# Kernel optimization log

Measured on AMD Instinct MI355X. Metric: run time of the kernel, lower is better.

Reference implementation:

```python
import jax, jax.numpy as jnp
import numpy as np

N = 50000      # nodes
E = 800000     # edges
IN_CH = 32
H = 64         # hidden_channels
OUT_CH = 16
L = 4          # num_layers
EPS = 1e-7     # GENConv message eps
LN_EPS = 1e-5


def _lin(key, fan_in, fan_out):
    kw, kb = jax.random.split(key)
    s = 1.0 / np.sqrt(fan_in)
    W = jax.random.uniform(kw, (fan_in, fan_out), jnp.float32, -s, s)
    b = jax.random.uniform(kb, (fan_out,), jnp.float32, -s, s)
    return W, b


def setup_inputs() -> dict:
    key = jax.random.key(0)
    ks = jax.random.split(key, 8)
    x = jax.random.normal(ks[0], (N, IN_CH), jnp.float32)
    edge_index = jax.random.randint(ks[1], (2, E), 0, N, dtype=jnp.int32)
    node_W, node_b = _lin(ks[2], IN_CH, H)
    W1, b1, W2, b2 = [], [], [], []
    for i in range(L):
        w1, bb1 = _lin(jax.random.fold_in(ks[3], i), H, 2 * H)
        w2, bb2 = _lin(jax.random.fold_in(ks[4], i), 2 * H, H)
        W1.append(w1); b1.append(bb1); W2.append(w2); b2.append(bb2)
    inp = {
        "x": x,
        "node_W": node_W, "node_b": node_b,
        "W1": jnp.stack(W1), "b1": jnp.stack(b1),          # [L,H,2H],[L,2H]
        "mlp_ln_g": jnp.ones((L, 2 * H), jnp.float32),      # LayerNorm inside GENConv MLP
        "mlp_ln_b": jnp.zeros((L, 2 * H), jnp.float32),
        "W2": jnp.stack(W2), "b2": jnp.stack(b2),          # [L,2H,H],[L,H]
        "t": jnp.ones((L,), jnp.float32),                   # learnable softmax temperature
        "ln_g": jnp.ones((L, H), jnp.float32),              # DeepGCNLayer LayerNorms
        "ln_b": jnp.zeros((L, H), jnp.float32),
        "edge_index": edge_index,
    }
    gW, gb = _lin(ks[5], H, OUT_CH)
    nW, nb = _lin(ks[6], H, OUT_CH + 1)
    inp.update({"g_W": gW, "g_b": gb, "n_W": nW, "n_b": nb})
    return inp


def _layer_norm(h, g, b):
    mu = h.mean(-1, keepdims=True)
    var = ((h - mu) ** 2).mean(-1, keepdims=True)
    return (h - mu) * jax.lax.rsqrt(var + LN_EPS) * g + b


def _gen_conv(h, src, dst, W1, b1, lg, lb, W2, b2, t):
    # message: relu(x_j) + eps  -> [E, H]
    m = jax.nn.relu(h[src]) + EPS
    # per-destination, per-channel scatter softmax with temperature t
    z = t * m
    zmax = jax.ops.segment_max(z, dst, num_segments=N)
    zmax = jnp.where(jnp.isfinite(zmax), zmax, 0.0)  # empty segments -> -inf
    a = jnp.exp(z - zmax[dst])
    denom = jax.ops.segment_sum(a, dst, num_segments=N)
    agg = jax.ops.segment_sum(m * a, dst, num_segments=N) / jnp.maximum(denom, EPS)
    out = agg + h  # root add
    # MLP [H, 2H, H] with LayerNorm + ReLU between
    u = jax.nn.relu(_layer_norm(out @ W1 + b1, lg, lb))
    return u @ W2 + b2


def reference(x, node_W, node_b, W1, b1, mlp_ln_g, mlp_ln_b, W2, b2, t,
              ln_g, ln_b, g_W, g_b, n_W, n_b, edge_index):
    src, dst = edge_index[0], edge_index[1]
    h = x @ node_W + node_b  # node encoder
    # first layer: conv only
    h = _gen_conv(h, src, dst, W1[0], b1[0], mlp_ln_g[0], mlp_ln_b[0], W2[0], b2[0], t[0])
    # remaining res+ blocks: x + conv(relu(norm(x)))  (dropout identity in eval)
    for i in range(1, L):
        y = jax.nn.relu(_layer_norm(h, ln_g[i], ln_b[i]))
        h = h + _gen_conv(y, src, dst, W1[i], b1[i], mlp_ln_g[i], mlp_ln_b[i], W2[i], b2[i], t[i])
    h = jax.nn.relu(_layer_norm(h, ln_g[0], ln_b[0]))
    g_out = jnp.max(h @ g_W + g_b, axis=0)   # batch=None -> global max over nodes
    n_out = h @ n_W + n_b
    return g_out, n_out
```

## Files before the change

kernel.cpp:

```cpp
#include <hip/hip_runtime.h>

#define NN 50000
#define NE 800000
#define INC 32
#define HH 64
#define H2 128
#define OC 16
#define ON 17
#define NL 4
#define MEPS 1e-7f
#define LNE 1e-5f
#define SCAN_BLOCKS 196
#define NLB ((NN + 127) / 128)
#define NBW ((NL * H2 * HH + 255) / 256)
#define NBH ((NE + 255) / 256)
#define NBE ((NN + 3) / 4)

typedef __attribute__((ext_vector_type(8))) short bf16x8;
typedef __attribute__((ext_vector_type(4))) float f32x4;

__device__ __forceinline__ unsigned short f2b(float x) {
    unsigned b = __float_as_uint(x);
    b += 0x7FFFu + ((b >> 16) & 1u);
    return (unsigned short)(b >> 16);
}
__device__ __forceinline__ float b2f(unsigned short u) {
    return __uint_as_float(((unsigned)u) << 16);
}

__global__ __launch_bounds__(256) void k_pre(
    const float* __restrict__ W1, const float* __restrict__ W2,
    const float* __restrict__ nW, const float* __restrict__ gW,
    const float* __restrict__ nbp, const float* __restrict__ gb,
    unsigned short* __restrict__ w1h, unsigned short* __restrict__ w1l,
    unsigned short* __restrict__ w2h, unsigned short* __restrict__ w2l,
    unsigned short* __restrict__ whh, unsigned short* __restrict__ whl,
    float* __restrict__ bc,
    const int* __restrict__ edst, int* __restrict__ counts, int* __restrict__ rank,
    const float* __restrict__ x, const float* __restrict__ nodeW,
    const float* __restrict__ nodeB, float* __restrict__ h,
    unsigned short* __restrict__ hbf)
{
    __shared__ float Ws[INC * HH];
    __shared__ float bs[HH];
    int bid = blockIdx.x, tid = threadIdx.x;
    if (bid < NBW) {
        int i = bid * 256 + tid;
        if (i < 48 * 64) {
            int j = i >> 6, k = i & 63;
            float v = 0.f;
            if (j < ON) v = nW[k * ON + j];
            else if (j < 33) v = gW[k * OC + (j - ON)];
            unsigned short hi = f2b(v);
            whh[i] = hi;
            whl[i] = f2b(v - b2f(hi));
        }
        if (i < 48) bc[i] = (i < ON) ? nbp[i] : ((i < 33) ? gb[i - ON] : 0.f);
        if (i >= NL * H2 * HH) return;
        int l = i / (H2 * HH), r = i % (H2 * HH);
        {
            int c = r / HH, k = r % HH;
            float v = W1[(size_t)l * HH * H2 + (size_t)k * H2 + c];
            unsigned short hi = f2b(v);
            w1h[i] = hi;
            w1l[i] = f2b(v - b2f(hi));
        }
        {
            int c = r / H2, k = r % H2;
            float v = W2[(size_t)l * H2 * HH + (size_t)k * HH + c];
            unsigned short hi = f2b(v);
            w2h[i] = hi;
            w2l[i] = f2b(v - b2f(hi));
        }
        return;
    }
    if (bid < NBW + NBH) {
        int e = (bid - NBW) * 256 + tid;
        if (e < NE) rank[e] = atomicAdd(&counts[edst[e]], 1);
        return;
    }
    for (int i = tid; i < INC * HH; i += 256) Ws[i] = nodeW[i];
    if (tid < HH) bs[tid] = nodeB[tid];
    __syncthreads();
    int wid = tid >> 6, lane = tid & 63;
    int n = (bid - NBW - NBH) * 4 + wid;
    if (n >= NN) return;
    float v = (lane < INC) ? x[(size_t)n * INC + lane] : 0.f;
    float acc = bs[lane];
    #pragma unroll
    for (int k = 0; k < INC; ++k)
        acc += __shfl(v, k) * Ws[k * HH + lane];
    h[(size_t)n * HH + lane] = acc;
    hbf[(size_t)n * HH + lane] = f2b(acc);
}

__global__ __launch_bounds__(256) void k_scan1(const int* __restrict__ counts,
                                               int* __restrict__ incl, int* __restrict__ bsums) {
    __shared__ int s[256];
    int t = threadIdx.x;
    int i = blockIdx.x * 256 + t;
    int v = (i < NN) ? counts[i] : 0;
    s[t] = v;
    __syncthreads();
    for (int off = 1; off < 256; off <<= 1) {
        int x = (t >= off) ? s[t - off] : 0;
        __syncthreads();
        s[t] += x;
        __syncthreads();
    }
    if (i < NN) incl[i] = s[t];
    if (t == 255) bsums[blockIdx.x] = s[255];
}

__global__ __launch_bounds__(256) void k_scan23(const int* __restrict__ counts,
                                                int* __restrict__ rowst, const int* __restrict__ bsums,
                                                int2* __restrict__ meta) {
    __shared__ int s[256];
    int t = threadIdx.x;
    int v = (t < SCAN_BLOCKS) ? bsums[t] : 0;
    s[t] = v;
    __syncthreads();
    for (int off = 1; off < 256; off <<= 1) {
        int x = (t >= off) ? s[t - off] : 0;
        __syncthreads();
        s[t] += x;
        __syncthreads();
    }
    int ex = s[t] - v;
    __syncthreads();
    s[t] = ex;
    __syncthreads();
    int pref = s[blockIdx.x];
    int i = blockIdx.x * 256 + t;
    if (i < NN) {
        int st = rowst[i] - counts[i] + pref;
        rowst[i] = st;
        meta[i] = make_int2(st, counts[i]);
    }
}

__global__ __launch_bounds__(256) void k_scatter2(const int* __restrict__ src, const int* __restrict__ dst,
                                                  const int* __restrict__ rank, const int* __restrict__ rowst,
                                                  int* __restrict__ ssrc) {
    int e = blockIdx.x * 256 + threadIdx.x;
    if (e < NE) ssrc[rowst[dst[e]] + rank[e]] = src[e];
}

__global__ __launch_bounds__(512, 4) void k_layer(
    const float* __restrict__ yin, const unsigned short* __restrict__ ybf_in,
    const int2* __restrict__ meta, const int* __restrict__ ssrc, const float* __restrict__ tp,
    const unsigned short* __restrict__ w1h, const unsigned short* __restrict__ w1l,
    const float* __restrict__ b1,
    const float* __restrict__ mlg, const float* __restrict__ mlb,
    const unsigned short* __restrict__ w2h, const unsigned short* __restrict__ w2l,
    const float* __restrict__ b2,
    const float* __restrict__ hres, float* __restrict__ hout,
    const float* __restrict__ lng1, const float* __restrict__ lnb1,
    float* __restrict__ yout, unsigned short* __restrict__ ybf_out,
    const float* __restrict__ lngF, const float* __restrict__ lnbF,
    const unsigned short* __restrict__ whh, const unsigned short* __restrict__ whl,
    const float* __restrict__ bc, float* __restrict__ dout, float* __restrict__ gmax)
{
    __shared__ __align__(16) unsigned short R1[2 * 128 * 68];
    __shared__ __align__(16) unsigned short R2[2 * 128 * 72];
    __shared__ float smax[8][16];
    unsigned short* aghS = R1;
    unsigned short* aglS = R1 + 128 * 68;
    unsigned short* W2hS = R1;
    unsigned short* W2lS = R1 + 128 * 68;
    bool last = (lng1 == nullptr);
    int tid = threadIdx.x;
    int w = tid >> 6, lane = tid & 63;
    int nl = lane & 15, g = lane >> 4;
    int nodeM = blockIdx.x * 128 + w * 16 + nl;
    bool validM = nodeM < NN;
    float tval = *tp;

    #pragma unroll
    for (int it = 0; it < 2; ++it) {
        int c = tid + it * 512;
        int row = c >> 3, col = (c & 7) << 3;
        float4 vh = *(const float4*)(w1h + c * 8);
        float4 vl = *(const float4*)(w1l + c * 8);
        *(float4*)&R2[row * 72 + col] = vh;
        *(float4*)&R2[9216 + row * 72 + col] = vl;
    }

    {
        int half = lane >> 5, l = lane & 31;
        for (int p = 0; p < 8; ++p) {
            int ln = p * 16 + w * 2 + half;
            int n = blockIdx.x * 128 + ln;
            bool valid = n < NN;
            int2 m = valid ? meta[n] : make_int2(0, 0);
            int start = m.x, deg = m.y;
            int dA = __shfl(deg, 0), dB = __shfl(deg, 32);
            int dmax = max(dA, dB);
            float Sa0 = 0.f, Sm0 = 0.f, Sa1 = 0.f, Sm1 = 0.f;
            for (int win = 0; win < dmax; win += 64) {
                int wcnt = min(64, dmax - win);
                int idxLo = (win + l < deg) ? ssrc[start + win + l] : 0;
                int idxHi = (win + 32 + l < deg) ? ssrc[start + win + 32 + l] : 0;
                for (int e0 = 0; e0 < wcnt; e0 += 8) {
                    float c0[8], c1[8];
                    int ev[8];
                    #pragma unroll
                    for (int i = 0; i < 8; ++i) {
                        int e = e0 + i;
                        ev[i] = win + e;
                        int sel = (e < 32) ? idxLo : idxHi;
                        int s = __shfl(sel, (lane & 32) | (e & 31));
                        unsigned vv = *(const unsigned*)(ybf_in + (size_t)s * HH + l * 2);
                        c0[i] = b2f((unsigned short)(vv & 0xffffu));
                        c1[i] = b2f((unsigned short)(vv >> 16));
                    }
                    #pragma unroll
                    for (int i = 0; i < 8; ++i) {
                        bool ok = ev[i] < deg;
                        float m0 = fmaxf(c0[i], 0.f) + MEPS;
                        float m1 = fmaxf(c1[i], 0.f) + MEPS;
                        float a0 = ok ? __expf(tval * m0) : 0.f;
                        float a1 = ok ? __expf(tval * m1) : 0.f;
                        Sa0 += a0; Sm0 += m0 * a0;
                        Sa1 += a1; Sm1 += m1 * a1;
                    }
                }
            }
            float av0 = 0.f, av1 = 0.f;
            if (valid) {
                float2 yv = *(const float2*)(yin + (size_t)n * HH + l * 2);
                av0 = Sm0 / fmaxf(Sa0, MEPS) + yv.x;
                av1 = Sm1 / fmaxf(Sa1, MEPS) + yv.y;
            }
            unsigned short h0 = f2b(av0), h1 = f2b(av1);
            ushort2 ph = {h0, h1};
            ushort2 pl = {f2b(av0 - b2f(h0)), f2b(av1 - b2f(h1))};
            *(ushort2*)&aghS[ln * 68 + 2 * l] = ph;
            *(ushort2*)&aglS[ln * 68 + 2 * l] = pl;
        }
    }
    __syncthreads();

    int lnM = w * 16 + nl;
    bf16x8 bAh[2], bAl[2];
    #pragma unroll
    for (int kc = 0; kc < 2; ++kc) {
        bAh[kc] = *(const bf16x8*)&aghS[lnM * 68 + kc * 32 + g * 8];
        bAl[kc] = *(const bf16x8*)&aglS[lnM * 68 + kc * 32 + g * 8];
    }
    f32x4 accU[8];
    #pragma unroll
    for (int t = 0; t < 8; ++t) {
        int uc = t * 16 + g * 4;
        float4 bb = *(const float4*)(b1 + uc);
        f32x4 a = {bb.x, bb.y, bb.z, bb.w};
        #pragma unroll
        for (int kc = 0; kc < 2; ++kc) {
            int wo = (t * 16 + nl) * 72 + kc * 32 + g * 8;
            bf16x8 ah = *(const bf16x8*)&R2[wo];
            bf16x8 al = *(const bf16x8*)&R2[9216 + wo];
            a = __builtin_amdgcn_mfma_f32_16x16x32_bf16(ah, bAh[kc], a, 0, 0, 0);
            a = __builtin_amdgcn_mfma_f32_16x16x32_bf16(al, bAh[kc], a, 0, 0, 0);
            a = __builtin_amdgcn_mfma_f32_16x16x32_bf16(ah, bAl[kc], a, 0, 0, 0);
        }
        accU[t] = a;
    }

    float s = 0.f, sq = 0.f;
    #pragma unroll
    for (int t = 0; t < 8; ++t) {
        #pragma unroll
        for (int j = 0; j < 4; ++j) { float v = accU[t][j]; s += v; sq += v * v; }
    }
    s += __shfl_xor(s, 16); sq += __shfl_xor(sq, 16);
    s += __shfl_xor(s, 32); sq += __shfl_xor(sq, 32);
    float mu = s * (1.f / 128.f);
    float var = sq * (1.f / 128.f) - mu * mu;
    float rs = rsqrtf(fmaxf(var, 0.f) + LNE);

    __syncthreads();

    #pragma unroll
    for (int it = 0; it < 2; ++it) {
        int c = tid + it * 512;
        int row = c >> 4, col = (c & 15) << 3;
        float4 vh = *(const float4*)(w2h + c * 8);
        float4 vl = *(const float4*)(w2l + c * 8);
        *(float4*)&W2hS[row * 136 + col] = vh;
        *(float4*)&W2lS[row * 136 + col] = vl;
    }
    unsigned short* myUt = R2 + w * (16 * 136);
    #pragma unroll
    for (int t = 0; t < 8; ++t) {
        int uc = t * 16 + g * 4;
        float4 gg = *(const float4*)(mlg + uc);
        float4 bb = *(const float4*)(mlb + uc);
        ushort4 pk;
        pk.x = f2b(fmaxf((accU[t][0] - mu) * rs * gg.x + bb.x, 0.f));
        pk.y = f2b(fmaxf((accU[t][1] - mu) * rs * gg.y + bb.y, 0.f));
        pk.z = f2b(fmaxf((accU[t][2] - mu) * rs * gg.z + bb.z, 0.f));
        pk.w = f2b(fmaxf((accU[t][3] - mu) * rs * gg.w + bb.w, 0.f));
        *(ushort4*)(&myUt[nl * 136 + uc]) = pk;
    }
    __syncthreads();

    bf16x8 bB[4];
    #pragma unroll
    for (int kc = 0; kc < 4; ++kc)
        bB[kc] = *(const bf16x8*)(&myUt[nl * 136 + kc * 32 + g * 8]);
    f32x4 accO[4];
    #pragma unroll
    for (int ot = 0; ot < 4; ++ot) {
        int oc = ot * 16 + g * 4;
        float4 bb = *(const float4*)(b2 + oc);
        f32x4 a = {bb.x, bb.y, bb.z, bb.w};
        #pragma unroll
        for (int kc = 0; kc < 4; ++kc) {
            int wo = (ot * 16 + nl) * 136 + kc * 32 + g * 8;
            bf16x8 ah = *(const bf16x8*)&W2hS[wo];
            bf16x8 al = *(const bf16x8*)&W2lS[wo];
            a = __builtin_amdgcn_mfma_f32_16x16x32_bf16(ah, bB[kc], a, 0, 0, 0);
            a = __builtin_amdgcn_mfma_f32_16x16x32_bf16(al, bB[kc], a, 0, 0, 0);
        }
        accO[ot] = a;
    }

    float4 oo[4];
    #pragma unroll
    for (int ot = 0; ot < 4; ++ot) {
        int oc = ot * 16 + g * 4;
        float4 o;
        o.x = accO[ot][0]; o.y = accO[ot][1]; o.z = accO[ot][2]; o.w = accO[ot][3];
        if (validM && hres) {
            float4 hr = *(const float4*)(hres + (size_t)nodeM * HH + oc);
            o.x += hr.x; o.y += hr.y; o.z += hr.z; o.w += hr.w;
        }
        oo[ot] = o;
    }

    if (!last) {
        #pragma unroll
        for (int ot = 0; ot < 4; ++ot) {
            int oc = ot * 16 + g * 4;
            if (validM) *(float4*)(hout + (size_t)nodeM * HH + oc) = oo[ot];
        }
        float s2 = 0.f, sq2 = 0.f;
        #pragma unroll
        for (int ot = 0; ot < 4; ++ot) {
            s2 += oo[ot].x + oo[ot].y + oo[ot].z + oo[ot].w;
            sq2 += oo[ot].x * oo[ot].x + oo[ot].y * oo[ot].y
                 + oo[ot].z * oo[ot].z + oo[ot].w * oo[ot].w;
        }
        s2 += __shfl_xor(s2, 16); sq2 += __shfl_xor(sq2, 16);
        s2 += __shfl_xor(s2, 32); sq2 += __shfl_xor(sq2, 32);
        float mu2 = s2 * (1.f / 64.f);
        float var2 = sq2 * (1.f / 64.f) - mu2 * mu2;
        float rs2 = rsqrtf(fmaxf(var2, 0.f) + LNE);
        #pragma unroll
        for (int ot = 0; ot < 4; ++ot) {
            int oc = ot * 16 + g * 4;
            float4 gg = *(const float4*)(lng1 + oc);
            float4 bb = *(const float4*)(lnb1 + oc);
            float4 v;
            v.x = fmaxf((oo[ot].x - mu2) * rs2 * gg.x + bb.x, 0.f);
            v.y = fmaxf((oo[ot].y - mu2) * rs2 * gg.y + bb.y, 0.f);
            v.z = fmaxf((oo[ot].z - mu2) * rs2 * gg.z + bb.z, 0.f);
            v.w = fmaxf((oo[ot].w - mu2) * rs2 * gg.w + bb.w, 0.f);
            if (validM) {
                *(float4*)(yout + (size_t)nodeM * HH + oc) = v;
                ushort4 p;
                p.x = f2b(v.x); p.y = f2b(v.y); p.z = f2b(v.z); p.w = f2b(v.w);
                *(ushort4*)(ybf_out + (size_t)nodeM * HH + oc) = p;
            }
        }
        return;
    }

    float s2 = 0.f, sq2 = 0.f;
    #pragma unroll
    for (int ot = 0; ot < 4; ++ot) {
        s2 += oo[ot].x + oo[ot].y + oo[ot].z + oo[ot].w;
        sq2 += oo[ot].x * oo[ot].x + oo[ot].y * oo[ot].y
             + oo[ot].z * oo[ot].z + oo[ot].w * oo[ot].w;
    }
    s2 += __shfl_xor(s2, 16); sq2 += __shfl_xor(sq2, 16);
    s2 += __shfl_xor(s2, 32); sq2 += __shfl_xor(sq2, 32);
    float mu2 = s2 * (1.f / 64.f);
    float var2 = sq2 * (1.f / 64.f) - mu2 * mu2;
    float rs2 = rsqrtf(fmaxf(var2, 0.f) + LNE);

    union { bf16x8 v; unsigned short u[8]; } Bh[2], Bl[2];
    #pragma unroll
    for (int kc = 0; kc < 2; ++kc) {
        #pragma unroll
        for (int e = 0; e < 8; ++e) {
            int ot = kc * 2 + (e >> 2);
            int c = ot * 16 + g * 4 + (e & 3);
            float hv = (e & 3) == 0 ? oo[ot].x : ((e & 3) == 1 ? oo[ot].y : ((e & 3) == 2 ? oo[ot].z : oo[ot].w));
            float v = fmaxf((hv - mu2) * rs2 * lngF[c] + lnbF[c], 0.f);
            unsigned short hi = f2b(v);
            Bh[kc].u[e] = hi;
            Bl[kc].u[e] = f2b(v - b2f(hi));
        }
    }
    f32x4 acc[3];
    #pragma unroll
    for (int t = 0; t < 3; ++t) {
        int j0 = t * 16 + g * 4;
        float4 bb = *(const float4*)(bc + j0);
        f32x4 a = {bb.x, bb.y, bb.z, bb.w};
        #pragma unroll
        for (int kc = 0; kc < 2; ++kc) {
            union { bf16x8 v; unsigned short u[8]; } Ah, Al;
            #pragma unroll
            for (int e = 0; e < 8; ++e) {
                int ot = kc * 2 + (e >> 2);
                int c = ot * 16 + g * 4 + (e & 3);
                Ah.u[e] = whh[(size_t)(t * 16 + nl) * 64 + c];
                Al.u[e] = whl[(size_t)(t * 16 + nl) * 64 + c];
            }
            a = __builtin_amdgcn_mfma_f32_16x16x32_bf16(Ah.v, Bh[kc].v, a, 0, 0, 0);
            a = __builtin_amdgcn_mfma_f32_16x16x32_bf16(Al.v, Bh[kc].v, a, 0, 0, 0);
            a = __builtin_amdgcn_mfma_f32_16x16x32_bf16(Ah.v, Bl[kc].v, a, 0, 0, 0);
        }
        acc[t] = a;
    }

    #pragma unroll
    for (int t = 0; t < 3; ++t) {
        #pragma unroll
        for (int reg = 0; reg < 4; ++reg) {
            int j = t * 16 + g * 4 + reg;
            float val = acc[t][reg];
            if (j < ON) {
                if (validM) dout[OC + (size_t)nodeM * ON + j] = val;
            } else if (j < 33) {
                float gv = validM ? val : -INFINITY;
                #pragma unroll
                for (int m = 1; m < 16; m <<= 1) gv = fmaxf(gv, __shfl_xor(gv, m));
                if (nl == 0) smax[w][j - ON] = gv;
            }
        }
    }
    __syncthreads();
    if (tid < 16) {
        float mm = -INFINITY;
        #pragma unroll
        for (int ww = 0; ww < 8; ++ww) mm = fmaxf(mm, smax[ww][tid]);
        gmax[(size_t)blockIdx.x * 16 + tid] = mm;
    }
}

__global__ void k_gdec(const float* __restrict__ gmax, float* __restrict__ dout) {
    int lane = threadIdx.x & 63;
    int ch = lane & 15, grp = lane >> 4;
    float m = -INFINITY;
    for (int b = grp; b < NLB; b += 4) m = fmaxf(m, gmax[(size_t)b * 16 + ch]);
    m = fmaxf(m, __shfl_xor(m, 16));
    m = fmaxf(m, __shfl_xor(m, 32));
    if (lane < 16) dout[ch] = m;
}

extern "C" void kernel_launch(void* const* d_in, const int* in_sizes, int n_in,
                              void* d_out, int out_size, void* d_ws, size_t ws_size,
                              hipStream_t stream) {
    const float* x     = (const float*)d_in[0];
    const float* nodeW = (const float*)d_in[1];
    const float* nodeB = (const float*)d_in[2];
    const float* W1    = (const float*)d_in[3];
    const float* b1    = (const float*)d_in[4];
    const float* mlg   = (const float*)d_in[5];
    const float* mlb   = (const float*)d_in[6];
    const float* W2    = (const float*)d_in[7];
    const float* b2    = (const float*)d_in[8];
    const float* tt    = (const float*)d_in[9];
    const float* lng   = (const float*)d_in[10];
    const float* lnb   = (const float*)d_in[11];
    const int*   ei    = (const int*)d_in[12];
    const float* gW    = (const float*)d_in[13];
    const float* gb    = (const float*)d_in[14];
    const float* nW    = (const float*)d_in[15];
    const float* nbp   = (const float*)d_in[16];
    float* out = (float*)d_out;

    char* ws = (char*)d_ws;
    size_t off = 0;
    auto alloc = [&](size_t bytes) -> void* {
        void* p = ws + off;
        off = (off + bytes + 255) & ~(size_t)255;
        return p;
    };
    int* counts    = (int*)alloc((size_t)NN * 4);
    size_t zero_end = off;
    float* gmax = (float*)alloc((size_t)NLB * 16 * 4);
    int* bsums = (int*)alloc(1024);
    int* rowst = (int*)alloc((size_t)NN * 4);
    int2* meta = (int2*)alloc((size_t)NN * 8);
    int* ssrc  = (int*)alloc((size_t)NE * 4);
    float* h   = (float*)alloc((size_t)NN * HH * 4);
    float* y   = (float*)alloc((size_t)NN * HH * 4);
    unsigned short* ybf0 = (unsigned short*)alloc((size_t)NN * HH * 2);
    unsigned short* ybf1 = (unsigned short*)alloc((size_t)NN * HH * 2);
    unsigned short* w1h = (unsigned short*)alloc((size_t)NL * H2 * HH * 2);
    unsigned short* w1l = (unsigned short*)alloc((size_t)NL * H2 * HH * 2);
    unsigned short* w2h = (unsigned short*)alloc((size_t)NL * H2 * HH * 2);
    unsigned short* w2l = (unsigned short*)alloc((size_t)NL * H2 * HH * 2);
    unsigned short* whh = (unsigned short*)alloc((size_t)48 * 64 * 2);
    unsigned short* whl = (unsigned short*)alloc((size_t)48 * 64 * 2);
    float* bc = (float*)alloc(48 * 4);
    int* rank = (int*)ybf1;

    const int* esrc = ei;
    const int* edst = ei + NE;

    hipMemsetAsync(d_ws, 0, zero_end, stream);

    k_pre<<<NBW + NBH + NBE, 256, 0, stream>>>(W1, W2, nW, gW, nbp, gb,
                                               w1h, w1l, w2h, w2l, whh, whl, bc,
                                               edst, counts, rank,
                                               x, nodeW, nodeB, h, ybf0);
    k_scan1<<<SCAN_BLOCKS, 256, 0, stream>>>(counts, rowst, bsums);
    k_scan23<<<SCAN_BLOCKS, 256, 0, stream>>>(counts, rowst, bsums, meta);
    k_scatter2<<<(NE + 255) / 256, 256, 0, stream>>>(esrc, edst, rank, rowst, ssrc);

    unsigned short* bufs[2] = {ybf0, ybf1};
    for (int l = 0; l < NL; ++l) {
        const float* yin = (l == 0) ? h : y;
        unsigned short* bin = bufs[l & 1];
        unsigned short* bout = bufs[(l + 1) & 1];
        bool lastL = (l == NL - 1);
        const float* ln1g = lastL ? nullptr : (lng + (size_t)(l + 1) * HH);
        const float* ln1b = lastL ? nullptr : (lnb + (size_t)(l + 1) * HH);
        k_layer<<<NLB, 512, 0, stream>>>(yin, bin, meta, ssrc, tt + l,
                                         w1h + (size_t)l * H2 * HH, w1l + (size_t)l * H2 * HH,
                                         b1 + (size_t)l * H2,
                                         mlg + (size_t)l * H2, mlb + (size_t)l * H2,
                                         w2h + (size_t)l * H2 * HH, w2l + (size_t)l * H2 * HH,
                                         b2 + (size_t)l * HH,
                                         (l == 0) ? (const float*)nullptr : h, h,
                                         ln1g, ln1b, y, bout,
                                         lng, lnb, whh, whl, bc, out, gmax);
    }
    k_gdec<<<1, 64, 0, stream>>>(gmax, out);
}
```

Before: 424.3 us.

## Split fused layer kernel into separate aggregation and MLP kernels

Each layer's fused gather-softmax-aggregate plus MLP kernel is split in two. A small-block aggregation kernel writes the hi/lo bf16 split of agg+root to global buffers, and an MLP kernel reads them back. The aim is higher occupancy and better latency hiding for the irregular gather, which is no longer tied to the 512-thread, LDS-heavy MLP block. The cost is an extra global round trip of the aggregated features, one more launch per layer, and a single ybf buffer instead of ping-pong.

```diff
diff --git a/kernel.cpp b/kernel.cpp
--- a/kernel.cpp
+++ b/kernel.cpp
@@ -11,7 +11,7 @@
 #define MEPS 1e-7f
 #define LNE 1e-5f
 #define SCAN_BLOCKS 196
-#define NLB ((NN + 127) / 128)
+#define NMB ((NN + 127) / 128)
 #define NBW ((NL * H2 * HH + 255) / 256)
 #define NBH ((NE + 255) / 256)
 #define NBE ((NN + 3) / 4)
@@ -146,9 +146,72 @@
     if (e < NE) ssrc[rowst[dst[e]] + rank[e]] = src[e];
 }
 
-__global__ __launch_bounds__(512, 4) void k_layer(
-    const float* __restrict__ yin, const unsigned short* __restrict__ ybf_in,
-    const int2* __restrict__ meta, const int* __restrict__ ssrc, const float* __restrict__ tp,
+__global__ __launch_bounds__(256) void k_agg(const float* __restrict__ y,
+                                             const unsigned short* __restrict__ ybf,
+                                             const int2* __restrict__ meta,
+                                             const int* __restrict__ ssrc,
+                                             const float* __restrict__ tp,
+                                             unsigned short* __restrict__ agh,
+                                             unsigned short* __restrict__ agl) {
+    int tid = threadIdx.x;
+    int w = tid >> 6, lane = tid & 63;
+    int half = lane >> 5;
+    int l = lane & 31;
+    int col = l;
+    int n = blockIdx.x * 8 + w * 2 + half;
+    bool valid = n < NN;
+    float tval = *tp;
+    int2 m = valid ? meta[n] : make_int2(0, 0);
+    int start = m.x, deg = m.y;
+
+    int dA = __shfl(deg, 0), dB = __shfl(deg, 32);
+    int dmax = max(dA, dB);
+
+    float Sa0 = 0.f, Sm0 = 0.f, Sa1 = 0.f, Sm1 = 0.f;
+    for (int win = 0; win < dmax; win += 64) {
+        int wcnt = min(64, dmax - win);
+        int idxLo = (win + l < deg) ? ssrc[start + win + l] : 0;
+        int idxHi = (win + 32 + l < deg) ? ssrc[start + win + 32 + l] : 0;
+        for (int e0 = 0; e0 < wcnt; e0 += 8) {
+            float c0[8], c1[8];
+            int ev[8];
+            #pragma unroll
+            for (int i = 0; i < 8; ++i) {
+                int e = e0 + i;
+                ev[i] = win + e;
+                int sel = (e < 32) ? idxLo : idxHi;
+                int s = __shfl(sel, (lane & 32) | (e & 31));
+                unsigned v = *(const unsigned*)(ybf + (size_t)s * HH + col * 2);
+                c0[i] = b2f((unsigned short)(v & 0xffffu));
+                c1[i] = b2f((unsigned short)(v >> 16));
+            }
+            #pragma unroll
+            for (int i = 0; i < 8; ++i) {
+                bool ok = ev[i] < deg;
+                float m0 = fmaxf(c0[i], 0.f) + MEPS;
+                float m1 = fmaxf(c1[i], 0.f) + MEPS;
+                float a0 = ok ? __expf(tval * m0) : 0.f;
+                float a1 = ok ? __expf(tval * m1) : 0.f;
+                Sa0 += a0; Sm0 += m0 * a0;
+                Sa1 += a1; Sm1 += m1 * a1;
+            }
+        }
+    }
+    if (!valid) return;
+    float agg0 = Sm0 / fmaxf(Sa0, MEPS);
+    float agg1 = Sm1 / fmaxf(Sa1, MEPS);
+    float2 yv = *(const float2*)(y + (size_t)n * HH + col * 2);
+    float av0 = agg0 + yv.x;
+    float av1 = agg1 + yv.y;
+    unsigned short h0 = f2b(av0), h1 = f2b(av1);
+    ushort2 ph = {h0, h1};
+    ushort2 pl = {f2b(av0 - b2f(h0)), f2b(av1 - b2f(h1))};
+    *(ushort2*)(agh + (size_t)n * HH + col * 2) = ph;
+    *(ushort2*)(agl + (size_t)n * HH + col * 2) = pl;
+}
+
+__global__ __launch_bounds__(512, 4) void k_mlp(
+    const unsigned short* __restrict__ agh, const unsigned short* __restrict__ agl,
     const unsigned short* __restrict__ w1h, const unsigned short* __restrict__ w1l,
     const float* __restrict__ b1,
     const float* __restrict__ mlg, const float* __restrict__ mlb,
@@ -156,25 +219,36 @@
     const float* __restrict__ b2,
     const float* __restrict__ hres, float* __restrict__ hout,
     const float* __restrict__ lng1, const float* __restrict__ lnb1,
-    float* __restrict__ yout, unsigned short* __restrict__ ybf_out,
+    float* __restrict__ y, unsigned short* __restrict__ ybf,
     const float* __restrict__ lngF, const float* __restrict__ lnbF,
     const unsigned short* __restrict__ whh, const unsigned short* __restrict__ whl,
     const float* __restrict__ bc, float* __restrict__ dout, float* __restrict__ gmax)
 {
-    __shared__ __align__(16) unsigned short R1[2 * 128 * 68];
-    __shared__ __align__(16) unsigned short R2[2 * 128 * 72];
+    __shared__ __align__(16) unsigned short W1S[2 * 128 * 72];
+    __shared__ __align__(16) unsigned short W2hS[64 * 136];
+    __shared__ __align__(16) unsigned short W2lS[64 * 136];
     __shared__ float smax[8][16];
-    unsigned short* aghS = R1;
-    unsigned short* aglS = R1 + 128 * 68;
-    unsigned short* W2hS = R1;
-    unsigned short* W2lS = R1 + 128 * 68;
     bool last = (lng1 == nullptr);
     int tid = threadIdx.x;
     int w = tid >> 6, lane = tid & 63;
     int nl = lane & 15, g = lane >> 4;
-    int nodeM = blockIdx.x * 128 + w * 16 + nl;
-    bool validM = nodeM < NN;
-    float tval = *tp;
+    int node = blockIdx.x * 128 + w * 16 + nl;
+    bool valid = node < NN;
+
+    bf16x8 bAh[2], bAl[2];
+    {
+        bf16x8 z = {0, 0, 0, 0, 0, 0, 0, 0};
+        if (valid) {
+            const unsigned short* rp = agh + (size_t)node * HH + g * 8;
+            bAh[0] = *(const bf16x8*)rp;
+            bAh[1] = *(const bf16x8*)(rp + 32);
+            const unsigned short* rq = agl + (size_t)node * HH + g * 8;
+            bAl[0] = *(const bf16x8*)rq;
+            bAl[1] = *(const bf16x8*)(rq + 32);
+        } else {
+            bAh[0] = z; bAh[1] = z; bAl[0] = z; bAl[1] = z;
+        }
+    }
 
     #pragma unroll
     for (int it = 0; it < 2; ++it) {
@@ -182,104 +256,9 @@
         int row = c >> 3, col = (c & 7) << 3;
         float4 vh = *(const float4*)(w1h + c * 8);
         float4 vl = *(const float4*)(w1l + c * 8);
-        *(float4*)&R2[row * 72 + col] = vh;
-        *(float4*)&R2[9216 + row * 72 + col] = vl;
-    }
-
-    {
-        int half = lane >> 5, l = lane & 31;
-        for (int p = 0; p < 8; ++p) {
-            int ln = p * 16 + w * 2 + half;
-            int n = blockIdx.x * 128 + ln;
-            bool valid = n < NN;
-            int2 m = valid ? meta[n] : make_int2(0, 0);
-            int start = m.x, deg = m.y;
-            int dA = __shfl(deg, 0), dB = __shfl(deg, 32);
-            int dmax = max(dA, dB);
-            float Sa0 = 0.f, Sm0 = 0.f, Sa1 = 0.f, Sm1 = 0.f;
-            for (int win = 0; win < dmax; win += 64) {
-                int wcnt = min(64, dmax - win);
-                int idxLo = (win + l < deg) ? ssrc[start + win + l] : 0;
-                int idxHi = (win + 32 + l < deg) ? ssrc[start + win + 32 + l] : 0;
-                for (int e0 = 0; e0 < wcnt; e0 += 8) {
-                    float c0[8], c1[8];
-                    int ev[8];
-                    #pragma unroll
-                    for (int i = 0; i < 8; ++i) {
-                        int e = e0 + i;
-                        ev[i] = win + e;
-                        int sel = (e < 32) ? idxLo : idxHi;
-                        int s = __shfl(sel, (lane & 32) | (e & 31));
-                        unsigned vv = *(const unsigned*)(ybf_in + (size_t)s * HH + l * 2);
-                        c0[i] = b2f((unsigned short)(vv & 0xffffu));
-                        c1[i] = b2f((unsigned short)(vv >> 16));
-                    }
-                    #pragma unroll
-                    for (int i = 0; i < 8; ++i) {
-                        bool ok = ev[i] < deg;
-                        float m0 = fmaxf(c0[i], 0.f) + MEPS;
-                        float m1 = fmaxf(c1[i], 0.f) + MEPS;
-                        float a0 = ok ? __expf(tval * m0) : 0.f;
-                        float a1 = ok ? __expf(tval * m1) : 0.f;
-                        Sa0 += a0; Sm0 += m0 * a0;
-                        Sa1 += a1; Sm1 += m1 * a1;
-                    }
-                }
-            }
-            float av0 = 0.f, av1 = 0.f;
-            if (valid) {
-                float2 yv = *(const float2*)(yin + (size_t)n * HH + l * 2);
-                av0 = Sm0 / fmaxf(Sa0, MEPS) + yv.x;
-                av1 = Sm1 / fmaxf(Sa1, MEPS) + yv.y;
-            }
-            unsigned short h0 = f2b(av0), h1 = f2b(av1);
-            ushort2 ph = {h0, h1};
-            ushort2 pl = {f2b(av0 - b2f(h0)), f2b(av1 - b2f(h1))};
-            *(ushort2*)&aghS[ln * 68 + 2 * l] = ph;
-            *(ushort2*)&aglS[ln * 68 + 2 * l] = pl;
-        }
-    }
-    __syncthreads();
-
-    int lnM = w * 16 + nl;
-    bf16x8 bAh[2], bAl[2];
-    #pragma unroll
-    for (int kc = 0; kc < 2; ++kc) {
-        bAh[kc] = *(const bf16x8*)&aghS[lnM * 68 + kc * 32 + g * 8];
-        bAl[kc] = *(const bf16x8*)&aglS[lnM * 68 + kc * 32 + g * 8];
-    }
-    f32x4 accU[8];
-    #pragma unroll
-    for (int t = 0; t < 8; ++t) {
-        int uc = t * 16 + g * 4;
-        float4 bb = *(const float4*)(b1 + uc);
-        f32x4 a = {bb.x, bb.y, bb.z, bb.w};
-        #pragma unroll
-        for (int kc = 0; kc < 2; ++kc) {
-            int wo = (t * 16 + nl) * 72 + kc * 32 + g * 8;
-            bf16x8 ah = *(const bf16x8*)&R2[wo];
-            bf16x8 al = *(const bf16x8*)&R2[9216 + wo];
-            a = __builtin_amdgcn_mfma_f32_16x16x32_bf16(ah, bAh[kc], a, 0, 0, 0);
-            a = __builtin_amdgcn_mfma_f32_16x16x32_bf16(al, bAh[kc], a, 0, 0, 0);
-            a = __builtin_amdgcn_mfma_f32_16x16x32_bf16(ah, bAl[kc], a, 0, 0, 0);
-        }
-        accU[t] = a;
-    }
-
-    float s = 0.f, sq = 0.f;
-    #pragma unroll
-    for (int t = 0; t < 8; ++t) {
-        #pragma unroll
-        for (int j = 0; j < 4; ++j) { float v = accU[t][j]; s += v; sq += v * v; }
-    }
-    s += __shfl_xor(s, 16); sq += __shfl_xor(sq, 16);
-    s += __shfl_xor(s, 32); sq += __shfl_xor(sq, 32);
-    float mu = s * (1.f / 128.f);
-    float var = sq * (1.f / 128.f) - mu * mu;
-    float rs = rsqrtf(fmaxf(var, 0.f) + LNE);
-
-    __syncthreads();
-
+        *(float4*)&W1S[row * 72 + col] = vh;
+        *(float4*)&W1S[9216 + row * 72 + col] = vl;
+    }
     #pragma unroll
     for (int it = 0; it < 2; ++it) {
         int c = tid + it * 512;
@@ -289,7 +268,41 @@
         *(float4*)&W2hS[row * 136 + col] = vh;
         *(float4*)&W2lS[row * 136 + col] = vl;
     }
-    unsigned short* myUt = R2 + w * (16 * 136);
+    __syncthreads();
+
+    f32x4 accU[8];
+    #pragma unroll
+    for (int t = 0; t < 8; ++t) {
+        int uc = t * 16 + g * 4;
+        float4 bb = *(const float4*)(b1 + uc);
+        f32x4 a = {bb.x, bb.y, bb.z, bb.w};
+        #pragma unroll
+        for (int kc = 0; kc < 2; ++kc) {
+            int wo = (t * 16 + nl) * 72 + kc * 32 + g * 8;
+            bf16x8 ah = *(const bf16x8*)&W1S[wo];
+            bf16x8 al = *(const bf16x8*)&W1S[9216 + wo];
+            a = __builtin_amdgcn_mfma_f32_16x16x32_bf16(ah, bAh[kc], a, 0, 0, 0);
+            a = __builtin_amdgcn_mfma_f32_16x16x32_bf16(al, bAh[kc], a, 0, 0, 0);
+            a = __builtin_amdgcn_mfma_f32_16x16x32_bf16(ah, bAl[kc], a, 0, 0, 0);
+        }
+        accU[t] = a;
+    }
+
+    float s = 0.f, sq = 0.f;
+    #pragma unroll
+    for (int t = 0; t < 8; ++t) {
+        #pragma unroll
+        for (int j = 0; j < 4; ++j) { float v = accU[t][j]; s += v; sq += v * v; }
+    }
+    s += __shfl_xor(s, 16); sq += __shfl_xor(sq, 16);
+    s += __shfl_xor(s, 32); sq += __shfl_xor(sq, 32);
+    float mu = s * (1.f / 128.f);
+    float var = sq * (1.f / 128.f) - mu * mu;
+    float rs = rsqrtf(fmaxf(var, 0.f) + LNE);
+
+    __syncthreads();
+    unsigned short* myUt = W1S + w * (16 * 136);
+
     #pragma unroll
     for (int t = 0; t < 8; ++t) {
         int uc = t * 16 + g * 4;
@@ -302,12 +315,13 @@
         pk.w = f2b(fmaxf((accU[t][3] - mu) * rs * gg.w + bb.w, 0.f));
         *(ushort4*)(&myUt[nl * 136 + uc]) = pk;
     }
-    __syncthreads();
+    asm volatile("s_waitcnt lgkmcnt(0)" ::: "memory");
 
     bf16x8 bB[4];
     #pragma unroll
     for (int kc = 0; kc < 4; ++kc)
         bB[kc] = *(const bf16x8*)(&myUt[nl * 136 + kc * 32 + g * 8]);
+
     f32x4 accO[4];
     #pragma unroll
     for (int ot = 0; ot < 4; ++ot) {
@@ -331,31 +345,32 @@
         int oc = ot * 16 + g * 4;
         float4 o;
         o.x = accO[ot][0]; o.y = accO[ot][1]; o.z = accO[ot][2]; o.w = accO[ot][3];
-        if (validM && hres) {
-            float4 hr = *(const float4*)(hres + (size_t)nodeM * HH + oc);
+        if (valid && hres) {
+            float4 hr = *(const float4*)(hres + (size_t)node * HH + oc);
             o.x += hr.x; o.y += hr.y; o.z += hr.z; o.w += hr.w;
         }
         oo[ot] = o;
     }
+
+    float s2 = 0.f, sq2 = 0.f;
+    #pragma unroll
+    for (int ot = 0; ot < 4; ++ot) {
+        s2 += oo[ot].x + oo[ot].y + oo[ot].z + oo[ot].w;
+        sq2 += oo[ot].x * oo[ot].x + oo[ot].y * oo[ot].y
+             + oo[ot].z * oo[ot].z + oo[ot].w * oo[ot].w;
+    }
+    s2 += __shfl_xor(s2, 16); sq2 += __shfl_xor(sq2, 16);
+    s2 += __shfl_xor(s2, 32); sq2 += __shfl_xor(sq2, 32);
+    float mu2 = s2 * (1.f / 64.f);
+    float var2 = sq2 * (1.f / 64.f) - mu2 * mu2;
+    float rs2 = rsqrtf(fmaxf(var2, 0.f) + LNE);
 
     if (!last) {
         #pragma unroll
         for (int ot = 0; ot < 4; ++ot) {
             int oc = ot * 16 + g * 4;
-            if (validM) *(float4*)(hout + (size_t)nodeM * HH + oc) = oo[ot];
-        }
-        float s2 = 0.f, sq2 = 0.f;
-        #pragma unroll
-        for (int ot = 0; ot < 4; ++ot) {
-            s2 += oo[ot].x + oo[ot].y + oo[ot].z + oo[ot].w;
-            sq2 += oo[ot].x * oo[ot].x + oo[ot].y * oo[ot].y
-                 + oo[ot].z * oo[ot].z + oo[ot].w * oo[ot].w;
-        }
-        s2 += __shfl_xor(s2, 16); sq2 += __shfl_xor(sq2, 16);
-        s2 += __shfl_xor(s2, 32); sq2 += __shfl_xor(sq2, 32);
-        float mu2 = s2 * (1.f / 64.f);
-        float var2 = sq2 * (1.f / 64.f) - mu2 * mu2;
-        float rs2 = rsqrtf(fmaxf(var2, 0.f) + LNE);
+            if (valid) *(float4*)(hout + (size_t)node * HH + oc) = oo[ot];
+        }
         #pragma unroll
         for (int ot = 0; ot < 4; ++ot) {
             int oc = ot * 16 + g * 4;
@@ -366,28 +381,15 @@
             v.y = fmaxf((oo[ot].y - mu2) * rs2 * gg.y + bb.y, 0.f);
             v.z = fmaxf((oo[ot].z - mu2) * rs2 * gg.z + bb.z, 0.f);
             v.w = fmaxf((oo[ot].w - mu2) * rs2 * gg.w + bb.w, 0.f);
-            if (validM) {
-                *(float4*)(yout + (size_t)nodeM * HH + oc) = v;
+            if (valid) {
+                *(float4*)(y + (size_t)node * HH + oc) = v;
                 ushort4 p;
                 p.x = f2b(v.x); p.y = f2b(v.y); p.z = f2b(v.z); p.w = f2b(v.w);
-                *(ushort4*)(ybf_out + (size_t)nodeM * HH + oc) = p;
+                *(ushort4*)(ybf + (size_t)node * HH + oc) = p;
             }
         }
         return;
     }
-
-    float s2 = 0.f, sq2 = 0.f;
-    #pragma unroll
-    for (int ot = 0; ot < 4; ++ot) {
-        s2 += oo[ot].x + oo[ot].y + oo[ot].z + oo[ot].w;
-        sq2 += oo[ot].x * oo[ot].x + oo[ot].y * oo[ot].y
-             + oo[ot].z * oo[ot].z + oo[ot].w * oo[ot].w;
-    }
-    s2 += __shfl_xor(s2, 16); sq2 += __shfl_xor(sq2, 16);
-    s2 += __shfl_xor(s2, 32); sq2 += __shfl_xor(sq2, 32);
-    float mu2 = s2 * (1.f / 64.f);
-    float var2 = sq2 * (1.f / 64.f) - mu2 * mu2;
-    float rs2 = rsqrtf(fmaxf(var2, 0.f) + LNE);
 
     union { bf16x8 v; unsigned short u[8]; } Bh[2], Bl[2];
     #pragma unroll
@@ -433,9 +435,9 @@
             int j = t * 16 + g * 4 + reg;
             float val = acc[t][reg];
             if (j < ON) {
-                if (validM) dout[OC + (size_t)nodeM * ON + j] = val;
+                if (valid) dout[OC + (size_t)node * ON + j] = val;
             } else if (j < 33) {
-                float gv = validM ? val : -INFINITY;
+                float gv = valid ? val : -INFINITY;
                 #pragma unroll
                 for (int m = 1; m < 16; m <<= 1) gv = fmaxf(gv, __shfl_xor(gv, m));
                 if (nl == 0) smax[w][j - ON] = gv;
@@ -455,7 +457,7 @@
     int lane = threadIdx.x & 63;
     int ch = lane & 15, grp = lane >> 4;
     float m = -INFINITY;
-    for (int b = grp; b < NLB; b += 4) m = fmaxf(m, gmax[(size_t)b * 16 + ch]);
+    for (int b = grp; b < NMB; b += 4) m = fmaxf(m, gmax[(size_t)b * 16 + ch]);
     m = fmaxf(m, __shfl_xor(m, 16));
     m = fmaxf(m, __shfl_xor(m, 32));
     if (lane < 16) dout[ch] = m;
@@ -492,15 +494,16 @@
     };
     int* counts    = (int*)alloc((size_t)NN * 4);
     size_t zero_end = off;
-    float* gmax = (float*)alloc((size_t)NLB * 16 * 4);
+    float* gmax = (float*)alloc((size_t)NMB * 16 * 4);
     int* bsums = (int*)alloc(1024);
     int* rowst = (int*)alloc((size_t)NN * 4);
     int2* meta = (int2*)alloc((size_t)NN * 8);
     int* ssrc  = (int*)alloc((size_t)NE * 4);
     float* h   = (float*)alloc((size_t)NN * HH * 4);
     float* y   = (float*)alloc((size_t)NN * HH * 4);
-    unsigned short* ybf0 = (unsigned short*)alloc((size_t)NN * HH * 2);
-    unsigned short* ybf1 = (unsigned short*)alloc((size_t)NN * HH * 2);
+    unsigned short* agh = (unsigned short*)alloc((size_t)NN * HH * 2);
+    unsigned short* agl = (unsigned short*)alloc((size_t)NN * HH * 2);
+    unsigned short* ybf = (unsigned short*)alloc((size_t)NN * HH * 2);
     unsigned short* w1h = (unsigned short*)alloc((size_t)NL * H2 * HH * 2);
     unsigned short* w1l = (unsigned short*)alloc((size_t)NL * H2 * HH * 2);
     unsigned short* w2h = (unsigned short*)alloc((size_t)NL * H2 * HH * 2);
@@ -508,7 +511,7 @@
     unsigned short* whh = (unsigned short*)alloc((size_t)48 * 64 * 2);
     unsigned short* whl = (unsigned short*)alloc((size_t)48 * 64 * 2);
     float* bc = (float*)alloc(48 * 4);
-    int* rank = (int*)ybf1;
+    int* rank = (int*)agh;
 
     const int* esrc = ei;
     const int* edst = ei + NE;
@@ -518,28 +521,26 @@
     k_pre<<<NBW + NBH + NBE, 256, 0, stream>>>(W1, W2, nW, gW, nbp, gb,
                                                w1h, w1l, w2h, w2l, whh, whl, bc,
                                                edst, counts, rank,
-                                               x, nodeW, nodeB, h, ybf0);
+                                               x, nodeW, nodeB, h, ybf);
     k_scan1<<<SCAN_BLOCKS, 256, 0, stream>>>(counts, rowst, bsums);
     k_scan23<<<SCAN_BLOCKS, 256, 0, stream>>>(counts, rowst, bsums, meta);
     k_scatter2<<<(NE + 255) / 256, 256, 0, stream>>>(esrc, edst, rank, rowst, ssrc);
 
-    unsigned short* bufs[2] = {ybf0, ybf1};
     for (int l = 0; l < NL; ++l) {
         const float* yin = (l == 0) ? h : y;
-        unsigned short* bin = bufs[l & 1];
-        unsigned short* bout = bufs[(l + 1) & 1];
+        k_agg<<<(NN + 7) / 8, 256, 0, stream>>>(yin, ybf, meta, ssrc, tt + l, agh, agl);
         bool lastL = (l == NL - 1);
         const float* ln1g = lastL ? nullptr : (lng + (size_t)(l + 1) * HH);
         const float* ln1b = lastL ? nullptr : (lnb + (size_t)(l + 1) * HH);
-        k_layer<<<NLB, 512, 0, stream>>>(yin, bin, meta, ssrc, tt + l,
-                                         w1h + (size_t)l * H2 * HH, w1l + (size_t)l * H2 * HH,
-                                         b1 + (size_t)l * H2,
-                                         mlg + (size_t)l * H2, mlb + (size_t)l * H2,
-                                         w2h + (size_t)l * H2 * HH, w2l + (size_t)l * H2 * HH,
-                                         b2 + (size_t)l * HH,
-                                         (l == 0) ? (const float*)nullptr : h, h,
-                                         ln1g, ln1b, y, bout,
-                                         lng, lnb, whh, whl, bc, out, gmax);
+        k_mlp<<<NMB, 512, 0, stream>>>(agh, agl,
+                                       w1h + (size_t)l * H2 * HH, w1l + (size_t)l * H2 * HH,
+                                       b1 + (size_t)l * H2,
+                                       mlg + (size_t)l * H2, mlb + (size_t)l * H2,
+                                       w2h + (size_t)l * H2 * HH, w2l + (size_t)l * H2 * HH,
+                                       b2 + (size_t)l * HH,
+                                       (l == 0) ? (const float*)nullptr : h, h,
+                                       ln1g, ln1b, y, ybf,
+                                       lng, lnb, whh, whl, bc, out, gmax);
     }
     k_gdec<<<1, 64, 0, stream>>>(gmax, out);
 }
```

Measured after the change: 376.3 us. 1.13x faster.
